# Kernel tuning notes

Hardware: AMD Instinct MI355X
Metric: run time of the kernel (lower is better)

## Reference

```python
import jax, jax.numpy as jnp
import numpy as np
import math

CHUNK = 32
NS_STEPS = 5
MAX_GNORM = 10.0


def _normalize(x, eps=1e-12):
    n = jnp.linalg.norm(x, axis=-1, keepdims=True)
    return x / jnp.maximum(n, eps)


def _poly(x):  # poly_degree = 2: [x, x^2] / sqrt(2)
    return jnp.concatenate([x, x * x], axis=-1) / math.sqrt(2.0)


def _ns5(G):
    # Muon-style Newton-Schulz orthogonalization (quintic, 5 steps)
    a, b, c = 3.4445, -4.7750, 2.0315
    t = G.shape[0] > G.shape[1]
    X = G.T if t else G
    X = X / (jnp.linalg.norm(X) + 1e-7)
    for _ in range(NS_STEPS):
        A = X @ X.T
        B = b * A + c * (A @ A)
        X = a * X + B @ X
    return X.T if t else X


def _clip_mean(g):
    # per-sample grad-norm clipping to MAX_GNORM, then mean over samples
    n = g.shape[0]
    norms = jnp.maximum(jnp.linalg.norm(g.reshape(n, -1), axis=1), 1e-8)
    scale = jnp.maximum(norms / MAX_GNORM, 1.0)
    return jnp.mean(g / scale.reshape((n,) + (1,) * (g.ndim - 1)), axis=0)


def _mem_fwd(W0, W1, z):  # MemoryMLP depth=2, gelu (exact) between layers
    return jax.nn.gelu(z @ W0, approximate=False) @ W1


def setup_inputs() -> dict:
    key = jax.random.key(0)
    ks = jax.random.split(key, 16)
    B, S, D, M, P, H = 2, 1024, 2048, 512, 1024, 2048
    w = lambda k, shape, fan_in: jax.random.normal(k, shape, jnp.float32) / np.float32(np.sqrt(fan_in))
    return {
        "x": jax.random.normal(ks[0], (B, S, D), jnp.float32),
        "Wk": w(ks[1], (M, D), D),
        "Wv": w(ks[2], (M, D), D),
        "Wq": w(ks[3], (M, D), D),
        "Wout": w(ks[4], (D, M), M),
        "w_lr": w(ks[5], (1, D), D), "b_lr": jnp.full((1,), -4.0, jnp.float32),
        "w_mom": w(ks[6], (1, D), D), "b_mom": jnp.full((1,), 1.0, jnp.float32),
        "w_dec": w(ks[7], (1, D), D), "b_dec": jnp.full((1,), -3.0, jnp.float32),
        "w_gate": w(ks[8], (1, D), D), "b_gate": jnp.full((1,), -1.0, jnp.float32),
        "Wmem0": w(ks[9], (P, H), P),
        "Wmem1": w(ks[10], (H, P), H),
        "Wmemout": w(ks[11], (P, M), P),
        "Wvexp": w(ks[12], (M, P), M),
    }


def reference(x, Wk, Wv, Wq, Wout, w_lr, b_lr, w_mom, b_mom, w_dec, b_dec,
              w_gate, b_gate, Wmem0, Wmem1, Wmemout, Wvexp):
    # Inference path (torch.is_grad_enabled() == False): chunked ATLAS update.
    B, S, D = x.shape
    NC = S // CHUNK

    k = _normalize(x @ Wk.T)          # (B,S,M)
    v = x @ Wv.T                       # (B,S,M)
    q = _normalize(x @ Wq.T)          # (B,S,M)
    kp = _poly(k)                      # (B,S,P)
    qp = _poly(q)                      # (B,S,P)
    vexp = v @ Wvexp                   # v_expand: (B,S,P)

    gate = lambda w, b: jax.nn.sigmoid(jnp.einsum('bsd,od->bso', x, w) + b)
    lr, mom, dec, og = gate(w_lr, b_lr), gate(w_mom, b_mom), gate(w_dec, b_dec), gate(w_gate, b_gate)

    cmean = lambda t: t[..., 0].reshape(B, NC, CHUNK).mean(axis=(0, 2))  # per-chunk scalar
    lr_c, mom_c, dec_c = cmean(lr), cmean(mom), cmean(dec)

    chunks = lambda t: t.reshape(B, NC, CHUNK, t.shape[-1]).transpose(1, 0, 2, 3)  # (NC,B,C,F)
    qc, kc, vc = chunks(qp), chunks(kp), chunks(vexp)

    def loss_fn(params, kk, vv):  # ||M(k) - v||^2 per sample
        W0_, W1_ = params
        pred = jax.nn.gelu(kk @ W0_, approximate=False) @ W1_
        return jnp.sum((pred - vv) ** 2)

    grad_fn = jax.vmap(jax.grad(loss_fn), in_axes=((None, None), 0, 0))

    def step(carry, xs):
        W0, W1, S0, S1 = carry
        qch, kch, vch, lrc, momc, decc = xs
        retr = _mem_fwd(W0, W1, qch) @ Wmemout  # retrieve with pre-update params: (B,C,M)
        kf = kch.reshape(-1, kch.shape[-1])
        vf = vch.reshape(-1, vch.shape[-1])
        g0, g1 = grad_fn((W0, W1), kf, vf)      # per-sample grads
        g0, g1 = _clip_mean(g0), _clip_mean(g1)
        s0 = momc * S0 - lrc * g0                # surprise momentum
        s1 = momc * S1 - lrc * g1
        W0n = (1.0 - decc) * W0 + _ns5(s0) * lrc # forget gate + orthogonalized step
        W1n = (1.0 - decc) * W1 + _ns5(s1) * lrc
        return (W0n, W1n, s0, s1), retr

    init = (Wmem0, Wmem1, jnp.zeros_like(Wmem0), jnp.zeros_like(Wmem1))
    _, retrs = jax.lax.scan(step, init, (qc, kc, vc, lr_c, mom_c, dec_c))
    retrieved = retrs.transpose(1, 0, 2, 3).reshape(B, S, -1)  # (B,S,M)
    delta = retrieved @ Wout.T
    return x + delta * og
```

## Files before the change

kernel.cpp:

```cpp
#include <hip/hip_runtime.h>


typedef unsigned short us;
typedef __attribute__((ext_vector_type(8))) short s16x8;
typedef __attribute__((ext_vector_type(8))) unsigned short u16x8;
typedef __attribute__((ext_vector_type(4))) float f32x4;

#define MKP 72

__device__ __forceinline__ float gelu_f(float x) {
  return 0.5f * x * (1.0f + erff(x * 0.70710678118654752f));
}
__device__ __forceinline__ float gelu_grad_f(float x) {
  float cdf = 0.5f * (1.0f + erff(x * 0.70710678118654752f));
  float pdf = 0.3989422804014327f * expf(-0.5f * x * x);
  return cdf + x * pdf;
}
__device__ __forceinline__ float sigmoid_f(float x) { return 1.0f / (1.0f + expf(-x)); }

__device__ __forceinline__ us f2bf(float f) {
  union { float f; unsigned u; } v; v.f = f;
  unsigned r = (v.u + 0x7FFFu + ((v.u >> 16) & 1u)) >> 16;
  return (us)r;
}
__device__ __forceinline__ float bf2f(us h) {
  union { unsigned u; float f; } v; v.u = ((unsigned)h) << 16;
  return v.f;
}
__device__ __forceinline__ int cm_map(int n) {
  return ((n & 1023) >> 5) * 64 + (n >> 10) * 32 + (n & 31);
}
__device__ __forceinline__ size_t pf_off(int r, int k, int KB) {
  return ((size_t)(r >> 4) * KB + (k >> 5)) * 512 + ((k >> 3) & 3) * 128 + (r & 15) * 8 + (k & 7);
}

__device__ __forceinline__ float block_reduce_sum(float v, float* red) {
  int t = threadIdx.x;
  red[t] = v; __syncthreads();
  for (int s = blockDim.x >> 1; s > 0; s >>= 1) {
    if (t < s) red[t] += red[t + s];
    __syncthreads();
  }
  float r = red[0];
  __syncthreads();
  return r;
}

__device__ __forceinline__ void gemm_pk(const us* __restrict__ A,
                                        const us* __restrict__ B, int KB,
                                        int lane, int m0, int n0,
                                        f32x4 (&acc)[4][4]) {
  const us* am[4];
  const us* bm[4];
#pragma unroll
  for (int q = 0; q < 4; ++q) {
    am[q] = A + (size_t)((m0 >> 4) + q) * KB * 512 + lane * 8;
    bm[q] = B + (size_t)((n0 >> 4) + q) * KB * 512 + lane * 8;
  }
#pragma unroll
  for (int i = 0; i < 4; ++i)
#pragma unroll
    for (int j = 0; j < 4; ++j) acc[i][j] = (f32x4){0.f, 0.f, 0.f, 0.f};
  u16x8 a0[4], b0[4], a1[4], b1[4];
#pragma unroll
  for (int q = 0; q < 4; ++q) {
    a0[q] = *(const u16x8*)(am[q]);
    b0[q] = *(const u16x8*)(bm[q]);
    a1[q] = *(const u16x8*)(am[q] + 512);
    b1[q] = *(const u16x8*)(bm[q] + 512);
  }
  for (int kb = 0; kb < KB; kb += 2) {
#pragma unroll
    for (int mi = 0; mi < 4; ++mi)
#pragma unroll
      for (int ni = 0; ni < 4; ++ni)
        acc[mi][ni] = __builtin_amdgcn_mfma_f32_16x16x32_bf16(
            (s16x8)a0[mi], (s16x8)b0[ni], acc[mi][ni], 0, 0, 0);
    if (kb + 2 < KB) {
#pragma unroll
      for (int q = 0; q < 4; ++q) {
        a0[q] = *(const u16x8*)(am[q] + (size_t)(kb + 2) * 512);
        b0[q] = *(const u16x8*)(bm[q] + (size_t)(kb + 2) * 512);
      }
    }
#pragma unroll
    for (int mi = 0; mi < 4; ++mi)
#pragma unroll
      for (int ni = 0; ni < 4; ++ni)
        acc[mi][ni] = __builtin_amdgcn_mfma_f32_16x16x32_bf16(
            (s16x8)a1[mi], (s16x8)b1[ni], acc[mi][ni], 0, 0, 0);
    if (kb + 3 < KB) {
#pragma unroll
      for (int q = 0; q < 4; ++q) {
        a1[q] = *(const u16x8*)(am[q] + (size_t)(kb + 3) * 512);
        b1[q] = *(const u16x8*)(bm[q] + (size_t)(kb + 3) * 512);
      }
    }
  }
}

template<int EPI, int TM, int TN>
__global__ __launch_bounds__(256)
void mgp_k(const us* __restrict__ Aq, const us* __restrict__ Bq,
           us* __restrict__ Cq, us* __restrict__ C2q, const us* __restrict__ Eq,
           int K, int N, float c1, float c2,
           long sA, long sB, long sC, long sE) {
  __shared__ __align__(16) us ct[4 * 64 * 72];
  const int tid = threadIdx.x;
  const int wave = tid >> 6, lane = tid & 63;
  const int l15 = lane & 15, l4 = lane >> 4;
  const int wm = (wave >> 1) * 64, wn = (wave & 1) * 64;
  const int TPB = TM * TN;
  const int t = blockIdx.x;
  const int bz = t / TPB;
  const int ti = t - bz * TPB;
  const int m0 = (ti / TN) * 128 + wm;
  const int n0 = (ti % TN) * 128 + wn;

  const us* A = Aq + (size_t)bz * sA;
  const us* B = Bq + (size_t)bz * sB;
  us* C = Cq + (size_t)bz * sC;
  us* C2 = C2q + (size_t)bz * sC;
  const us* E = Eq + (size_t)bz * sE;
  const int KB = K >> 5;

  f32x4 acc[4][4];
  gemm_pk(A, B, KB, lane, m0, n0, acc);

  us* cw = ct + wave * 64 * 72;
#pragma unroll
  for (int mi = 0; mi < 4; ++mi)
#pragma unroll
    for (int i = 0; i < 4; ++i)
#pragma unroll
      for (int ni = 0; ni < 4; ++ni)
        cw[(mi * 16 + l4 * 4 + i) * 72 + ni * 16 + l15] = f2bf(acc[mi][ni][i]);

  if constexpr (EPI == 20 || EPI == 21) {
    const int KC = N >> 5;
#pragma unroll
    for (int q = 0; q < 8; ++q) {
      u16x8 v = *(const u16x8*)&cw[lane * 72 + q * 8];
      size_t off = pf_off(m0 + lane, n0 + q * 8, KC);
      if constexpr (EPI == 21) {
        u16x8 e = *(const u16x8*)(E + off);
        u16x8 o;
#pragma unroll
        for (int w = 0; w < 8; ++w) o[w] = f2bf(c1 * bf2f(v[w]) + c2 * bf2f(e[w]));
        *(u16x8*)(C + off) = o;
      } else {
        *(u16x8*)(C + off) = v;
      }
    }
  } else if constexpr (EPI == 23) {
#pragma unroll
    for (int q = 0; q < 8; ++q) {
      size_t off = pf_off(m0 + lane, n0 + q * 8, 64);
      u16x8 v = *(const u16x8*)&cw[lane * 72 + q * 8];
      u16x8 e = *(const u16x8*)(E + off);
      u16x8 o;
#pragma unroll
      for (int w = 0; w < 8; ++w) o[w] = f2bf(bf2f(v[w]) + c1 * bf2f(e[w]));
      *(u16x8*)&cw[lane * 72 + q * 8] = o;
      *(u16x8*)(C + off) = o;
    }
#pragma unroll
    for (int q = 0; q < 8; ++q) {
      u16x8 o;
#pragma unroll
      for (int w = 0; w < 8; ++w) o[w] = cw[(q * 8 + w) * 72 + lane];
      size_t offT = pf_off(n0 + lane, m0 + q * 8, 32);
      *(u16x8*)(C2 + offT) = o;
    }
  } else {
#pragma unroll
    for (int q = 0; q < 8; ++q) {
      size_t off = pf_off(m0 + lane, n0 + q * 8, 64);
      u16x8 v = *(const u16x8*)&cw[lane * 72 + q * 8];
      u16x8 e = *(const u16x8*)(E + off);
      u16x8 o;
#pragma unroll
      for (int w = 0; w < 8; ++w) o[w] = f2bf(bf2f(v[w]) + c1 * bf2f(e[w]));
      *(u16x8*)(C + (size_t)(m0 + lane) * 2048 + n0 + q * 8) = o;
    }
  }
}

template<int EPI, int TM, int TN>
static void mgp(hipStream_t st, const us* A, const us* B, us* C, us* C2,
                const us* E, int K, int N, float c1, float c2,
                long sA, long sB, long sC, long sE) {
  dim3 g(TM * TN * 2), b(256);
  hipLaunchKernelGGL((mgp_k<EPI, TM, TN>), g, b, 0, st, A, B, C, C2, E,
                     K, N, c1, c2, sA, sB, sC, sE);
}

template<int EPI>
__device__ __forceinline__ void epilogue(f32x4 (&acc)[4][4], int m0, int n0,
    int l15, int l4, void* Cq, void* C2, const void* Eq,
    const float* FX, const float* OG, const float* cp, int cidx,
    int ldc, int lde, float c1, float c2) {
#pragma unroll
  for (int mi = 0; mi < 4; ++mi) {
#pragma unroll
    for (int i = 0; i < 4; ++i) {
      int grow = m0 + mi * 16 + l4 * 4 + i;
#pragma unroll
      for (int ni = 0; ni < 4; ++ni) {
        int col = n0 + ni * 16 + l15;
        float v = acc[mi][ni][i];
        if constexpr (EPI == 5) {
          ((us*)Cq)[(size_t)grow * ldc + col] = f2bf(v);
        } else if constexpr (EPI == 7) {
          ((float*)Cq)[(size_t)grow * ldc + col] = v;
        } else if constexpr (EPI == 8) {
          ((us*)Cq)[(size_t)grow * ldc + col] = f2bf(gelu_f(v));
          if (m0 >= 64)
            ((float*)C2)[(size_t)(grow - 64) * ldc + col] = gelu_grad_f(v);
        } else if constexpr (EPI == 9) {
          if (m0 < 64)
            ((us*)Cq)[(size_t)grow * ldc + col] = f2bf(v);
          else
            ((us*)Cq)[(size_t)grow * ldc + col] =
                f2bf(2.0f * (v - ((const float*)Eq)[(size_t)(grow - 64) * lde + col]));
        } else if constexpr (EPI == 13) {
          ((float*)Cq)[(size_t)grow * ldc + col] =
              v * ((const float*)Eq)[(size_t)grow * lde + col];
        } else if constexpr (EPI == 14) {
          float* C = (float*)Cq;
          float old = C[(size_t)grow * ldc + col];
          C[(size_t)grow * ldc + col] = cp[cidx * 3 + 1] * old - cp[cidx * 3 + 0] * v;
        } else if constexpr (EPI == 15) {
          ((float*)Cq)[(size_t)grow * ldc + col] =
              FX[(size_t)grow * ldc + col] + v * OG[grow];
        } else if constexpr (EPI == 17) {
          int crow = cm_map(grow);
          ((float*)Cq)[(size_t)crow * ldc + col] = v;
        }
      }
    }
  }
}

template<int EPI, int TA, int DUAL, int AG>
__device__ __forceinline__ void mg_body(const us* __restrict__ A0,
    const us* __restrict__ A2, const us* __restrict__ B,
    void* __restrict__ Cq, void* __restrict__ C2, const void* __restrict__ Eq,
    const float* __restrict__ FX, const float* __restrict__ OG,
    const float* __restrict__ cp, int cidx, int m0, int n0,
    int K, int lda, int ldb, int ldc, int lde, float c1, float c2,
    us* As, us* Bs, int t) {
  const us* A = A0;
  if constexpr (DUAL) { if (m0 >= 64) A = A2; }
  const int mA0 = DUAL ? (m0 & 63) : m0;
  const int l15 = t & 15, l4 = t >> 4;

  f32x4 acc[4][4];
#pragma unroll
  for (int i = 0; i < 4; ++i)
#pragma unroll
    for (int j = 0; j < 4; ++j) acc[i][j] = (f32x4){0.f, 0.f, 0.f, 0.f};

  const int srw = t >> 3;
  const int sck = (t & 7) * 8;

  u16x8 ra[8], rb[8];
  auto LDA = [&](int k0) {
#pragma unroll
    for (int p = 0; p < 8; ++p) {
      if constexpr (TA == 0) {
        int row = srw + p * 8;
        int srow;
        if constexpr (AG) srow = cm_map(m0 + row); else srow = mA0 + row;
        ra[p] = *(const u16x8*)(A + (size_t)srow * lda + k0 + sck);
      } else {
        ra[p] = *(const u16x8*)(A + (size_t)(k0 + srw + p * 8) * lda + mA0 + sck);
      }
    }
  };
  auto LDB = [&](int k0) {
#pragma unroll
    for (int p = 0; p < 8; ++p)
      rb[p] = *(const u16x8*)(B + (size_t)(n0 + srw + p * 8) * ldb + k0 + sck);
  };

  LDA(0); LDB(0);
  for (int k0 = 0; k0 < K; k0 += 64) {
    if constexpr (TA == 0) {
#pragma unroll
      for (int p = 0; p < 8; ++p)
        *(u16x8*)&As[(srw + p * 8) * MKP + sck] = ra[p];
    } else {
#pragma unroll
      for (int p = 0; p < 8; ++p) {
        int kk = srw + p * 8;
#pragma unroll
        for (int j = 0; j < 8; ++j) As[(sck + j) * MKP + kk] = ra[p][j];
      }
    }
#pragma unroll
    for (int p = 0; p < 8; ++p)
      *(u16x8*)&Bs[(srw + p * 8) * MKP + sck] = rb[p];
    if (k0 + 64 < K) { LDA(k0 + 64); LDB(k0 + 64); }
#pragma unroll
    for (int ks = 0; ks < 2; ++ks) {
      s16x8 af[4], bf[4];
#pragma unroll
      for (int mi = 0; mi < 4; ++mi)
        af[mi] = *(const s16x8*)&As[(mi * 16 + l15) * MKP + ks * 32 + l4 * 8];
#pragma unroll
      for (int ni = 0; ni < 4; ++ni)
        bf[ni] = *(const s16x8*)&Bs[(ni * 16 + l15) * MKP + ks * 32 + l4 * 8];
#pragma unroll
      for (int mi = 0; mi < 4; ++mi)
#pragma unroll
        for (int ni = 0; ni < 4; ++ni)
          acc[mi][ni] = __builtin_amdgcn_mfma_f32_16x16x32_bf16(af[mi], bf[ni], acc[mi][ni], 0, 0, 0);
    }
  }

  epilogue<EPI>(acc, m0, n0, l15, l4, Cq, C2, Eq, FX, OG, cp, cidx,
                ldc, lde, c1, c2);
}

template<int EPI, int TA, int DUAL, int AG>
__global__ __launch_bounds__(64)
void mg_k(const us* __restrict__ Aq, const us* __restrict__ A2,
          const us* __restrict__ Bq, void* __restrict__ Cq,
          void* __restrict__ C2, const void* __restrict__ Eq,
          const float* __restrict__ FX, const float* __restrict__ OG,
          const float* __restrict__ cp, int cidx,
          int M, int N, int K, int lda, int ldb, int ldc, int lde,
          float c1, float c2) {
  __shared__ __align__(16) us As[64 * MKP];
  __shared__ __align__(16) us Bs[64 * MKP];
  mg_body<EPI, TA, DUAL, AG>(Aq, A2, Bq, Cq, C2, Eq, FX, OG, cp, cidx,
                             blockIdx.y * 64, blockIdx.x * 64, K, lda, ldb,
                             ldc, lde, c1, c2, As, Bs, threadIdx.x);
}

template<int EPI, int TA = 0, int DUAL = 0, int AG = 0>
static void mg(hipStream_t st, const us* A, const us* A2, const us* B,
               void* C, void* C2, const void* E,
               const float* FX, const float* OG, const float* cp, int cidx,
               int M, int N, int K, int lda, int ldb, int ldc, int lde,
               float c1 = 0.f, float c2 = 0.f) {
  dim3 g(N / 64, M / 64, 1), b(64);
  hipLaunchKernelGGL((mg_k<EPI, TA, DUAL, AG>), g, b, 0, st, A, A2, B, C, C2, E,
                     FX, OG, cp, cidx, M, N, K, lda, ldb, ldc, lde, c1, c2);
}

__global__ __launch_bounds__(64)
void mg2_k(const us* __restrict__ kp_c, const us* __restrict__ dhT,
           float* __restrict__ S0, const us* __restrict__ habk,
           const us* __restrict__ rbwT, float* __restrict__ S1,
           const float* __restrict__ cp, int c) {
  __shared__ __align__(16) us As[64 * MKP];
  __shared__ __align__(16) us Bs[64 * MKP];
  int bid = blockIdx.x;
  if (bid < 512) {
    int m0 = (bid >> 5) * 64, n0 = (bid & 31) * 64;
    mg_body<14, 1, 0, 0>(kp_c, nullptr, dhT, S0, nullptr, nullptr,
                         nullptr, nullptr, cp, c, m0, n0,
                         64, 1024, 64, 2048, 0, 0.f, 0.f, As, Bs, threadIdx.x);
  } else {
    int b2 = bid - 512;
    int m0 = (b2 >> 4) * 64, n0 = (b2 & 15) * 64;
    mg_body<14, 1, 0, 0>(habk, nullptr, rbwT, S1, nullptr, nullptr,
                         nullptr, nullptr, cp, c, m0, n0,
                         64, 2048, 64, 1024, 0, 0.f, 0.f, As, Bs, threadIdx.x);
  }
}

__global__ void wt2_k(const float* __restrict__ dh, const float* __restrict__ w0inv,
                      us* __restrict__ dhT, const us* __restrict__ prg,
                      const float* __restrict__ w1inv, us* __restrict__ rbwT) {
  __shared__ float tile[32][33];
  int bid = blockIdx.x;
  int tx = threadIdx.x, ty = threadIdx.y;
  int c0, r0, ldin;
  const float* wv;
  us* outp;
  bool f32in;
  const void* in;
  if (bid < 128) {
    in = dh; wv = w0inv; outp = dhT; ldin = 2048; f32in = true;
    c0 = (bid & 63) * 32; r0 = (bid >> 6) * 32;
  } else {
    int b2 = bid - 128;
    in = prg; wv = w1inv; outp = rbwT; ldin = 1024; f32in = false;
    c0 = (b2 & 31) * 32; r0 = (b2 >> 5) * 32;
  }
#pragma unroll
  for (int j = 0; j < 4; ++j) {
    int r = r0 + ty + 8 * j, cc = c0 + tx;
    float v = f32in ? ((const float*)in)[(size_t)r * ldin + cc]
                    : bf2f(((const us*)in)[(size_t)r * ldin + cc]);
    tile[ty + 8 * j][tx] = v * wv[r];
  }
  __syncthreads();
#pragma unroll
  for (int j = 0; j < 4; ++j)
    outp[(size_t)(c0 + ty + 8 * j) * 64 + r0 + tx] = f2bf(tile[tx][ty + 8 * j]);
}

__global__ void scalepk2_k(const float* __restrict__ S0, const float* __restrict__ S1,
                           const float* __restrict__ inv01,
                           us* __restrict__ XP, us* __restrict__ XTP) {
  __shared__ float tile[32][33];
  const long SB2c = 2097152;
  int z = blockIdx.z;
  float s = inv01[z];
  int tx = threadIdx.x, ty = threadIdx.y;
  int r0, c0;
  const float* S;
  if (z == 0) { S = S0; c0 = blockIdx.x * 32; r0 = blockIdx.y * 32; }
  else        { S = S1; r0 = blockIdx.x * 32; c0 = blockIdx.y * 32; }
  int C = (z == 0) ? 2048 : 1024;
#pragma unroll
  for (int j = 0; j < 4; ++j)
    tile[ty + 8 * j][tx] = S[(size_t)(r0 + ty + 8 * j) * C + c0 + tx] * s;
  __syncthreads();
  us* xp = XP + (size_t)z * SB2c;
  us* xt = XTP + (size_t)z * SB2c;
  int t = ty * 32 + tx;
  if (t < 128) {
    int rh = t >> 2, cc = t & 3;
    u16x8 v;
#pragma unroll
    for (int e = 0; e < 8; ++e) v[e] = f2bf(tile[rh][cc * 8 + e]);
    if (z == 0) {
      *(u16x8*)(xp + pf_off(r0 + rh, c0 + cc * 8, 64)) = v;
    } else {
      *(u16x8*)(xt + pf_off(r0 + rh, c0 + cc * 8, 32)) = v;
    }
  } else {
    int ch = (t - 128) >> 2, rc = (t - 128) & 3;
    u16x8 v;
#pragma unroll
    for (int e = 0; e < 8; ++e) v[e] = f2bf(tile[rc * 8 + e][ch]);
    if (z == 0) {
      *(u16x8*)(xt + pf_off(c0 + ch, r0 + rc * 8, 32)) = v;
    } else {
      *(u16x8*)(xp + pf_off(c0 + ch, r0 + rc * 8, 64)) = v;
    }
  }
}


__global__ __launch_bounds__(256) void conv_k(const float* __restrict__ in,
                                              us* __restrict__ out, int n) {
  for (int i = blockIdx.x * 256 + threadIdx.x; i < n; i += gridDim.x * 256)
    out[i] = f2bf(in[i]);
}

__global__ void tconv_k(const float* __restrict__ in, us* __restrict__ out, int R, int C) {
  __shared__ float tile[32][33];
  int c0 = blockIdx.x * 32, r0 = blockIdx.y * 32;
  int tx = threadIdx.x, ty = threadIdx.y;
#pragma unroll
  for (int j = 0; j < 4; ++j)
    tile[ty + 8 * j][tx] = in[(size_t)(r0 + ty + 8 * j) * C + c0 + tx];
  __syncthreads();
#pragma unroll
  for (int j = 0; j < 4; ++j)
    out[(size_t)(c0 + ty + 8 * j) * R + r0 + tx] = f2bf(tile[tx][ty + 8 * j]);
}


__global__ __launch_bounds__(256) void polynorm2_k(const float* __restrict__ lin,
                                                   us* __restrict__ outp) {
  __shared__ float red[256];
  int n = blockIdx.x, t = threadIdx.x;
  int rowp = cm_map(n);
  float s = 0.f;
  for (int f = t; f < 512; f += 256) { float v = lin[(size_t)n * 512 + f]; s += v * v; }
  float tot = block_reduce_sum(s, red);
  float sc = 1.0f / fmaxf(sqrtf(tot), 1e-12f);
  const float is2 = 0.70710678118654752f;
  for (int f = t; f < 512; f += 256) {
    float v = lin[(size_t)n * 512 + f] * sc;
    outp[(size_t)rowp * 1024 + f] = f2bf(v * is2);
    outp[(size_t)rowp * 1024 + 512 + f] = f2bf(v * v * is2);
  }
}

__global__ __launch_bounds__(256) void gates_k(const float* __restrict__ x,
    const float* __restrict__ wlr, const float* __restrict__ blr,
    const float* __restrict__ wmom, const float* __restrict__ bmom,
    const float* __restrict__ wdec, const float* __restrict__ bdec,
    const float* __restrict__ wgate, const float* __restrict__ bgate,
    float* __restrict__ lrv, float* __restrict__ momv,
    float* __restrict__ decv, float* __restrict__ og) {
  __shared__ float red[256];
  int n = blockIdx.x, t = threadIdx.x;
  float s0 = 0.f, s1 = 0.f, s2 = 0.f, s3 = 0.f;
  for (int d = t; d < 2048; d += 256) {
    float xv = x[(size_t)n * 2048 + d];
    s0 += xv * wlr[d]; s1 += xv * wmom[d]; s2 += xv * wdec[d]; s3 += xv * wgate[d];
  }
  float r0 = block_reduce_sum(s0, red);
  float r1 = block_reduce_sum(s1, red);
  float r2 = block_reduce_sum(s2, red);
  float r3 = block_reduce_sum(s3, red);
  if (t == 0) {
    lrv[n] = sigmoid_f(r0 + blr[0]);
    momv[n] = sigmoid_f(r1 + bmom[0]);
    decv[n] = sigmoid_f(r2 + bdec[0]);
    og[n] = sigmoid_f(r3 + bgate[0]);
  }
}

__global__ void chunk_means_k(const float* __restrict__ lrv, const float* __restrict__ momv,
                              const float* __restrict__ decv, float* __restrict__ cp) {
  int c = blockIdx.x, t = threadIdx.x;
  int n = ((t >> 5) << 10) + c * 32 + (t & 31);
  float a = lrv[n], b = momv[n], d = decv[n];
  for (int off = 32; off > 0; off >>= 1) {
    a += __shfl_down(a, off);
    b += __shfl_down(b, off);
    d += __shfl_down(d, off);
  }
  if (t == 0) {
    cp[c * 3 + 0] = a * (1.f / 64.f);
    cp[c * 3 + 1] = b * (1.f / 64.f);
    cp[c * 3 + 2] = d * (1.f / 64.f);
  }
}

__global__ __launch_bounds__(256) void sampnorm2_k(const us* __restrict__ kp_b,
                                                   const float* __restrict__ dh,
                                                   const us* __restrict__ hab,
                                                   const us* __restrict__ pr,
                                                   float* __restrict__ w0inv,
                                                   float* __restrict__ w1inv, int c) {
  __shared__ float red[256];
  int i = blockIdx.x, t = threadIdx.x;
  int row = c * 64 + i;
  float sk = 0.f, sr = 0.f, sdh = 0.f, sa = 0.f;
  for (int p = t; p < 1024; p += 256) {
    float v = bf2f(kp_b[(size_t)row * 1024 + p]); sk += v * v;
    v = bf2f(pr[(size_t)(64 + i) * 1024 + p]); sr += v * v;
  }
  for (int h = t; h < 2048; h += 256) {
    float v = dh[(size_t)i * 2048 + h]; sdh += v * v;
    v = bf2f(hab[(size_t)(64 + i) * 2048 + h]); sa += v * v;
  }
  float tk = block_reduce_sum(sk, red);
  float tdh = block_reduce_sum(sdh, red);
  float ta = block_reduce_sum(sa, red);
  float tr = block_reduce_sum(sr, red);
  if (t == 0) {
    float n0 = fmaxf(sqrtf(tk) * sqrtf(tdh), 1e-8f);
    w0inv[i] = 1.0f / (64.0f * fmaxf(n0 * 0.1f, 1.0f));
    float n1 = fmaxf(sqrtf(ta) * sqrtf(tr), 1e-8f);
    w1inv[i] = 1.0f / (64.0f * fmaxf(n1 * 0.1f, 1.0f));
  }
}

__global__ __launch_bounds__(256) void frob2_k(const float* __restrict__ s0,
                                               const float* __restrict__ s1, int n,
                                               float* __restrict__ parts) {
  __shared__ float red[256];
  const float* s = blockIdx.z ? s1 : s0;
  float acc = 0.f;
  for (int i = blockIdx.x * 256 + threadIdx.x; i < n; i += gridDim.x * 256) {
    float v = s[i]; acc += v * v;
  }
  float r = block_reduce_sum(acc, red);
  if (threadIdx.x == 0) parts[blockIdx.z * 256 + blockIdx.x] = r;
}

__global__ __launch_bounds__(256) void frob_fin2_k(const float* __restrict__ parts,
                                                   float* __restrict__ inv) {
  __shared__ float red[256];
  float r = block_reduce_sum(parts[blockIdx.x * 256 + threadIdx.x], red);
  if (threadIdx.x == 0) inv[blockIdx.x] = 1.0f / (sqrtf(r) + 1e-7f);
}

__global__ void wupd0_k(float* __restrict__ W0, const us* __restrict__ X,
                        us* __restrict__ W0bT, const float* __restrict__ cp, int c) {
  __shared__ float tl[32][33];
  float lr = cp[c * 3 + 0], om = 1.0f - cp[c * 3 + 2];
  int c0 = blockIdx.x * 32, r0 = blockIdx.y * 32;
  int tx = threadIdx.x, ty = threadIdx.y;
#pragma unroll
  for (int j = 0; j < 4; ++j) {
    int r = r0 + ty + 8 * j, h = c0 + tx;
    size_t idx = (size_t)r * 2048 + h;
    float v = om * W0[idx] + lr * bf2f(X[idx]);
    W0[idx] = v;
    tl[ty + 8 * j][tx] = v;
  }
  __syncthreads();
#pragma unroll
  for (int j = 0; j < 4; ++j)
    W0bT[(size_t)(c0 + ty + 8 * j) * 1024 + r0 + tx] = f2bf(tl[tx][ty + 8 * j]);
}

__global__ void wupd1_k(float* __restrict__ W1, const us* __restrict__ X2,
                        us* __restrict__ W1b, us* __restrict__ W1bT,
                        const float* __restrict__ cp, int c) {
  __shared__ float tX[32][33];
  __shared__ float t2[32][33];
  float lr = cp[c * 3 + 0], om = 1.0f - cp[c * 3 + 2];
  int h0 = blockIdx.x * 32, p0 = blockIdx.y * 32;
  int tx = threadIdx.x, ty = threadIdx.y;
#pragma unroll
  for (int j = 0; j < 4; ++j)
    tX[ty + 8 * j][tx] = bf2f(X2[(size_t)(p0 + ty + 8 * j) * 2048 + h0 + tx]);
  __syncthreads();
#pragma unroll
  for (int j = 0; j < 4; ++j) {
    int h = h0 + ty + 8 * j, p = p0 + tx;
    size_t idx = (size_t)h * 1024 + p;
    float v = om * W1[idx] + lr * tX[tx][ty + 8 * j];
    W1[idx] = v;
    W1b[idx] = f2bf(v);
    t2[tx][ty + 8 * j] = v;
  }
  __syncthreads();
#pragma unroll
  for (int j = 0; j < 4; ++j)
    W1bT[(size_t)(p0 + ty + 8 * j) * 2048 + h0 + tx] = f2bf(t2[ty + 8 * j][tx]);
}


extern "C" void kernel_launch(void* const* d_in, const int* in_sizes, int n_in,
                              void* d_out, int out_size, void* d_ws, size_t ws_size,
                              hipStream_t stream) {
  const float* x = (const float*)d_in[0];
  const float* Wk = (const float*)d_in[1];
  const float* Wv = (const float*)d_in[2];
  const float* Wq = (const float*)d_in[3];
  const float* Wout = (const float*)d_in[4];
  const float* w_lr = (const float*)d_in[5];
  const float* b_lr = (const float*)d_in[6];
  const float* w_mom = (const float*)d_in[7];
  const float* b_mom = (const float*)d_in[8];
  const float* w_dec = (const float*)d_in[9];
  const float* b_dec = (const float*)d_in[10];
  const float* w_gate = (const float*)d_in[11];
  const float* b_gate = (const float*)d_in[12];
  const float* Wmem0 = (const float*)d_in[13];
  const float* Wmem1 = (const float*)d_in[14];
  const float* Wmemout = (const float*)d_in[15];
  const float* Wvexp = (const float*)d_in[16];
  float* out = (float*)d_out;
  (void)n_in; (void)in_sizes; (void)out_size;

  const long F = 1048576;
  const long BIG = 2097152;
  const long SB2 = 2097152, SB1 = 1048576;
  float* ws = (float*)d_ws;
  if (ws_size < (size_t)25043464 * sizeof(float)) return;

  us* kp_b   = (us*)ws;
  us* qp_b   = (us*)(ws + F);
  float* vexp = ws + 2 * F;
  float* W0  = ws + 4 * F;
  float* W1  = ws + 6 * F;
  float* S0  = ws + 8 * F;
  float* S1  = ws + 10 * F;
  us* XPong  = (us*)(ws + 12 * F);
  us* XTPong = (us*)(ws + 14 * F);
  us* XPing  = (us*)(ws + 16 * F);
  us* AP     = (us*)(ws + 18 * F);
  float* SCR = ws + 19 * F;
  us* XTPing = (us*)(ws + 20 * F);
  us* BP     = (us*)(ws + 22 * F);
  us* W0bT   = (us*)(ws + 20 * F);
  us* W1bT   = (us*)(ws + 21 * F);
  us* W1b    = (us*)(ws + 22 * F);
  us* WmoT   = (us*)(ws + 23 * F);
  us* retrv  = (us*)(ws + 23 * F + 262144);
  float* smal = ws + 23 * F + 262144 + 524288;
  float* og   = smal;
  float* lrv  = og + 2048;
  float* momv = lrv + 2048;
  float* decv = momv + 2048;
  float* cpb  = decv + 2048;
  float* w0inv = cpb + 128;
  float* w1inv = w0inv + 64;
  float* parts = w1inv + 64;
  float* inv01 = parts + 512;

  us* xb   = XPong;
  us* Wkb  = XTPong;
  us* Wqb  = XTPong + 1048576;
  us* Wvb  = XTPong + 2097152;
  us* vlin = XPing;
  us* WvexpT = XPing + 1048576;
  us* Woutb = AP;
  float* lin = SCR;
  us* hab   = (us*)SCR;
  float* gp = SCR + 131072;
  us* pr    = (us*)(SCR + 262144);
  float* dh = SCR + 327680;
  us* dhT   = (us*)(SCR + 458752);
  us* rbwT  = (us*)(SCR + 524288);
  us* Xfin  = XPong;

  const float NSa = 3.4445f, NSb = -4.7750f, NSc = 2.0315f;

  hipMemcpyAsync(W0, Wmem0, (size_t)BIG * 4, hipMemcpyDeviceToDevice, stream);
  hipMemcpyAsync(W1, Wmem1, (size_t)BIG * 4, hipMemcpyDeviceToDevice, stream);
  hipMemsetAsync(S0, 0, (size_t)BIG * 4, stream);
  hipMemsetAsync(S1, 0, (size_t)BIG * 4, stream);
  hipLaunchKernelGGL(tconv_k, dim3(64, 32), dim3(32, 8), 0, stream, Wmem0, W0bT, 1024, 2048);
  hipLaunchKernelGGL(conv_k, dim3(1024), dim3(256), 0, stream, Wmem1, W1b, (int)BIG);
  hipLaunchKernelGGL(tconv_k, dim3(32, 64), dim3(32, 8), 0, stream, Wmem1, W1bT, 2048, 1024);
  hipLaunchKernelGGL(tconv_k, dim3(16, 32), dim3(32, 8), 0, stream, Wmemout, WmoT, 1024, 512);
  hipLaunchKernelGGL(tconv_k, dim3(32, 16), dim3(32, 8), 0, stream, Wvexp, WvexpT, 512, 1024);
  hipLaunchKernelGGL(conv_k, dim3(2048), dim3(256), 0, stream, x, xb, 2048 * 2048);
  hipLaunchKernelGGL(conv_k, dim3(512), dim3(256), 0, stream, Wk, Wkb, 512 * 2048);
  hipLaunchKernelGGL(conv_k, dim3(512), dim3(256), 0, stream, Wq, Wqb, 512 * 2048);
  hipLaunchKernelGGL(conv_k, dim3(512), dim3(256), 0, stream, Wv, Wvb, 512 * 2048);

  mg<7>(stream, xb, nullptr, Wkb, lin, nullptr, nullptr, nullptr, nullptr, nullptr, 0,
        2048, 512, 2048, 2048, 2048, 512, 0);
  hipLaunchKernelGGL(polynorm2_k, dim3(2048), dim3(256), 0, stream, lin, kp_b);
  mg<7>(stream, xb, nullptr, Wqb, lin, nullptr, nullptr, nullptr, nullptr, nullptr, 0,
        2048, 512, 2048, 2048, 2048, 512, 0);
  hipLaunchKernelGGL(polynorm2_k, dim3(2048), dim3(256), 0, stream, lin, qp_b);
  mg<5>(stream, xb, nullptr, Wvb, vlin, nullptr, nullptr, nullptr, nullptr, nullptr, 0,
        2048, 512, 2048, 2048, 2048, 512, 0);
  mg<17>(stream, vlin, nullptr, WvexpT, vexp, nullptr, nullptr, nullptr, nullptr, nullptr, 0,
         2048, 1024, 512, 512, 512, 1024, 0);

  hipLaunchKernelGGL(gates_k, dim3(2048), dim3(256), 0, stream, x,
                     w_lr, b_lr, w_mom, b_mom, w_dec, b_dec, w_gate, b_gate,
                     lrv, momv, decv, og);
  hipLaunchKernelGGL(chunk_means_k, dim3(32), dim3(64), 0, stream, lrv, momv, decv, cpb);

  for (int c = 0; c < 32; ++c) {
    const us* kp_c = kp_b + (size_t)c * 64 * 1024;
    const us* qp_c = qp_b + (size_t)c * 64 * 1024;
    const float* vexp_c = vexp + (size_t)c * 64 * 1024;
    mg<8, 0, 1>(stream, qp_c, kp_c, W0bT, hab, gp, nullptr, nullptr, nullptr, nullptr, 0,
                128, 2048, 1024, 1024, 1024, 2048, 0);
    mg<9>(stream, hab, nullptr, W1bT, pr, nullptr, vexp_c, nullptr, nullptr, nullptr, 0,
          128, 1024, 2048, 2048, 2048, 1024, 1024);
    mg<5>(stream, pr, nullptr, WmoT, retrv + (size_t)c * 64 * 512, nullptr, nullptr,
          nullptr, nullptr, nullptr, 0, 64, 512, 1024, 1024, 1024, 512, 0);
    mg<13>(stream, pr + 64 * 1024, nullptr, W1b, dh, nullptr, gp, nullptr, nullptr, nullptr, 0,
           64, 2048, 1024, 1024, 1024, 2048, 2048);
    hipLaunchKernelGGL(sampnorm2_k, dim3(64), dim3(256), 0, stream,
                       kp_b, dh, hab, pr, w0inv, w1inv, c);
    hipLaunchKernelGGL(wt2_k, dim3(192), dim3(32, 8), 0, stream,
                       dh, w0inv, dhT, pr + 64 * 1024, w1inv, rbwT);
    hipLaunchKernelGGL(mg2_k, dim3(1024), dim3(64), 0, stream,
                       kp_c, dhT, S0, hab + 64 * 2048, rbwT, S1, cpb, c);

    hipLaunchKernelGGL(frob2_k, dim3(256, 1, 2), dim3(256), 0, stream, S0, S1, (int)BIG, parts);
    hipLaunchKernelGGL(frob_fin2_k, dim3(2), dim3(256), 0, stream, parts, inv01);
    hipLaunchKernelGGL(scalepk2_k, dim3(64, 32, 2), dim3(32, 8), 0, stream,
                       S0, S1, inv01, XPing, XTPing);

    us* xpA[2] = {XPing, XPong};
    us* xtA[2] = {XTPing, XTPong};
    int cur = 0;
    for (int it = 0; it < 5; ++it) {
      const us* XPc = xpA[cur];
      const us* XTPc = xtA[cur];
      int nxt = cur ^ 1;
      mgp<20, 8, 8>(stream, XPc, XPc, AP, nullptr, nullptr, 2048, 1024,
                    0.f, 0.f, SB2, SB2, SB1, 0);
      mgp<21, 8, 8>(stream, AP, AP, BP, nullptr, AP, 1024, 1024,
                    NSc, NSb, SB1, SB1, SB1, SB1);
      if (it < 4) {
        mgp<23, 8, 16>(stream, BP, XTPc, xpA[nxt], xtA[nxt], XPc, 1024, 2048,
                       NSa, 0.f, SB1, SB2, SB2, SB2);
        cur = nxt;
      } else {
        mgp<24, 8, 16>(stream, BP, XTPc, Xfin, nullptr, XPc, 1024, 2048,
                       NSa, 0.f, SB1, SB2, SB2, SB2);
      }
    }
    hipLaunchKernelGGL(wupd0_k, dim3(64, 32), dim3(32, 8), 0, stream, W0, Xfin, W0bT, cpb, c);
    hipLaunchKernelGGL(wupd1_k, dim3(64, 32), dim3(32, 8), 0, stream, W1, Xfin + SB2, W1b, W1bT, cpb, c);
  }

  hipLaunchKernelGGL(conv_k, dim3(1024), dim3(256), 0, stream, Wout, Woutb, 2048 * 512);
  mg<15, 0, 0, 1>(stream, retrv, nullptr, Woutb, out, nullptr, nullptr, x, og, nullptr, 0,
                  2048, 2048, 512, 512, 512, 2048, 0);
}
```

Before: 15.34 ms.

## Fuse Frobenius norm into momentum GEMM epilogue and merge small per-chunk launches

The momentum-update GEMM epilogue now accumulates the sum of squares of the new surprise values and writes one partial per block, so the separate full-matrix Frobenius reduction pass over S0/S1 is gone. The two small retrieval and dh GEMMs are merged into one launch with block-index dispatch, and the two weight-update kernels are combined into one launch over a z dimension. The aim is to cut per-chunk launch count and a redundant read of the large momentum buffers, at the cost of a small extra reduction in the GEMM tail.

Measured after the change: 14.31 ms (median of 2 runs). 6.7% less time.

```diff
diff --git a/kernel.cpp b/kernel.cpp
--- a/kernel.cpp
+++ b/kernel.cpp
@@ -196,10 +196,11 @@
 }
 
 template<int EPI>
-__device__ __forceinline__ void epilogue(f32x4 (&acc)[4][4], int m0, int n0,
+__device__ __forceinline__ float epilogue(f32x4 (&acc)[4][4], int m0, int n0,
     int l15, int l4, void* Cq, void* C2, const void* Eq,
     const float* FX, const float* OG, const float* cp, int cidx,
     int ldc, int lde, float c1, float c2) {
+  float ssq = 0.f;
 #pragma unroll
   for (int mi = 0; mi < 4; ++mi) {
 #pragma unroll
@@ -229,7 +230,9 @@
         } else if constexpr (EPI == 14) {
           float* C = (float*)Cq;
           float old = C[(size_t)grow * ldc + col];
-          C[(size_t)grow * ldc + col] = cp[cidx * 3 + 1] * old - cp[cidx * 3 + 0] * v;
+          float nv = cp[cidx * 3 + 1] * old - cp[cidx * 3 + 0] * v;
+          C[(size_t)grow * ldc + col] = nv;
+          ssq += nv * nv;
         } else if constexpr (EPI == 15) {
           ((float*)Cq)[(size_t)grow * ldc + col] =
               FX[(size_t)grow * ldc + col] + v * OG[grow];
@@ -240,10 +243,11 @@
       }
     }
   }
+  return ssq;
 }
 
 template<int EPI, int TA, int DUAL, int AG>
-__device__ __forceinline__ void mg_body(const us* __restrict__ A0,
+__device__ __forceinline__ float mg_body(const us* __restrict__ A0,
     const us* __restrict__ A2, const us* __restrict__ B,
     void* __restrict__ Cq, void* __restrict__ C2, const void* __restrict__ Eq,
     const float* __restrict__ FX, const float* __restrict__ OG,
@@ -319,8 +323,8 @@
     }
   }
 
-  epilogue<EPI>(acc, m0, n0, l15, l4, Cq, C2, Eq, FX, OG, cp, cidx,
-                ldc, lde, c1, c2);
+  return epilogue<EPI>(acc, m0, n0, l15, l4, Cq, C2, Eq, FX, OG, cp, cidx,
+                       ldc, lde, c1, c2);
 }
 
 template<int EPI, int TA, int DUAL, int AG>
@@ -354,21 +358,43 @@
 void mg2_k(const us* __restrict__ kp_c, const us* __restrict__ dhT,
            float* __restrict__ S0, const us* __restrict__ habk,
            const us* __restrict__ rbwT, float* __restrict__ S1,
-           const float* __restrict__ cp, int c) {
+           const float* __restrict__ cp, int c, float* __restrict__ parts2) {
   __shared__ __align__(16) us As[64 * MKP];
   __shared__ __align__(16) us Bs[64 * MKP];
   int bid = blockIdx.x;
+  float ssq;
   if (bid < 512) {
     int m0 = (bid >> 5) * 64, n0 = (bid & 31) * 64;
-    mg_body<14, 1, 0, 0>(kp_c, nullptr, dhT, S0, nullptr, nullptr,
-                         nullptr, nullptr, cp, c, m0, n0,
-                         64, 1024, 64, 2048, 0, 0.f, 0.f, As, Bs, threadIdx.x);
+    ssq = mg_body<14, 1, 0, 0>(kp_c, nullptr, dhT, S0, nullptr, nullptr,
+                               nullptr, nullptr, cp, c, m0, n0,
+                               64, 1024, 64, 2048, 0, 0.f, 0.f, As, Bs, threadIdx.x);
   } else {
     int b2 = bid - 512;
     int m0 = (b2 >> 4) * 64, n0 = (b2 & 15) * 64;
-    mg_body<14, 1, 0, 0>(habk, nullptr, rbwT, S1, nullptr, nullptr,
-                         nullptr, nullptr, cp, c, m0, n0,
-                         64, 2048, 64, 1024, 0, 0.f, 0.f, As, Bs, threadIdx.x);
+    ssq = mg_body<14, 1, 0, 0>(habk, nullptr, rbwT, S1, nullptr, nullptr,
+                               nullptr, nullptr, cp, c, m0, n0,
+                               64, 2048, 64, 1024, 0, 0.f, 0.f, As, Bs, threadIdx.x);
+  }
+  for (int off = 32; off > 0; off >>= 1) ssq += __shfl_down(ssq, off);
+  if (threadIdx.x == 0) parts2[bid] = ssq;
+}
+
+__global__ __launch_bounds__(64)
+void mg34_k(const us* __restrict__ pr, const us* __restrict__ WmoT,
+            us* __restrict__ retrv_c, const us* __restrict__ W1b,
+            float* __restrict__ dh, const float* __restrict__ gp) {
+  __shared__ __align__(16) us As[64 * MKP];
+  __shared__ __align__(16) us Bs[64 * MKP];
+  int bid = blockIdx.x;
+  if (bid < 8) {
+    mg_body<5, 0, 0, 0>(pr, nullptr, WmoT, retrv_c, nullptr, nullptr,
+                        nullptr, nullptr, nullptr, 0, 0, bid * 64,
+                        1024, 1024, 1024, 512, 0, 0.f, 0.f, As, Bs, threadIdx.x);
+  } else {
+    int b2 = bid - 8;
+    mg_body<13, 0, 0, 0>(pr + 64 * 1024, nullptr, W1b, dh, nullptr, gp,
+                         nullptr, nullptr, nullptr, 0, 0, b2 * 64,
+                         1024, 1024, 1024, 2048, 2048, 0.f, 0.f, As, Bs, threadIdx.x);
   }
 }
 
@@ -558,71 +584,57 @@
   }
 }
 
-__global__ __launch_bounds__(256) void frob2_k(const float* __restrict__ s0,
-                                               const float* __restrict__ s1, int n,
-                                               float* __restrict__ parts) {
-  __shared__ float red[256];
-  const float* s = blockIdx.z ? s1 : s0;
-  float acc = 0.f;
-  for (int i = blockIdx.x * 256 + threadIdx.x; i < n; i += gridDim.x * 256) {
-    float v = s[i]; acc += v * v;
-  }
-  float r = block_reduce_sum(acc, red);
-  if (threadIdx.x == 0) parts[blockIdx.z * 256 + blockIdx.x] = r;
-}
-
-__global__ __launch_bounds__(256) void frob_fin2_k(const float* __restrict__ parts,
-                                                   float* __restrict__ inv) {
-  __shared__ float red[256];
-  float r = block_reduce_sum(parts[blockIdx.x * 256 + threadIdx.x], red);
-  if (threadIdx.x == 0) inv[blockIdx.x] = 1.0f / (sqrtf(r) + 1e-7f);
-}
-
-__global__ void wupd0_k(float* __restrict__ W0, const us* __restrict__ X,
-                        us* __restrict__ W0bT, const float* __restrict__ cp, int c) {
-  __shared__ float tl[32][33];
+__global__ __launch_bounds__(512) void frob_fin512_k(const float* __restrict__ parts2,
+                                                     float* __restrict__ inv) {
+  __shared__ float red[512];
+  int z = blockIdx.x;
+  float r = block_reduce_sum(parts2[z * 512 + threadIdx.x], red);
+  if (threadIdx.x == 0) inv[z] = 1.0f / (sqrtf(r) + 1e-7f);
+}
+
+__global__ void wupd01_k(float* __restrict__ W0, const us* __restrict__ X0,
+                         us* __restrict__ W0bT,
+                         float* __restrict__ W1, const us* __restrict__ X2,
+                         us* __restrict__ W1b, us* __restrict__ W1bT,
+                         const float* __restrict__ cp, int c) {
+  __shared__ float tA[32][33];
+  __shared__ float tB[32][33];
   float lr = cp[c * 3 + 0], om = 1.0f - cp[c * 3 + 2];
-  int c0 = blockIdx.x * 32, r0 = blockIdx.y * 32;
   int tx = threadIdx.x, ty = threadIdx.y;
-#pragma unroll
-  for (int j = 0; j < 4; ++j) {
-    int r = r0 + ty + 8 * j, h = c0 + tx;
-    size_t idx = (size_t)r * 2048 + h;
-    float v = om * W0[idx] + lr * bf2f(X[idx]);
-    W0[idx] = v;
-    tl[ty + 8 * j][tx] = v;
-  }
-  __syncthreads();
-#pragma unroll
-  for (int j = 0; j < 4; ++j)
-    W0bT[(size_t)(c0 + ty + 8 * j) * 1024 + r0 + tx] = f2bf(tl[tx][ty + 8 * j]);
-}
-
-__global__ void wupd1_k(float* __restrict__ W1, const us* __restrict__ X2,
-                        us* __restrict__ W1b, us* __restrict__ W1bT,
-                        const float* __restrict__ cp, int c) {
-  __shared__ float tX[32][33];
-  __shared__ float t2[32][33];
-  float lr = cp[c * 3 + 0], om = 1.0f - cp[c * 3 + 2];
-  int h0 = blockIdx.x * 32, p0 = blockIdx.y * 32;
-  int tx = threadIdx.x, ty = threadIdx.y;
-#pragma unroll
-  for (int j = 0; j < 4; ++j)
-    tX[ty + 8 * j][tx] = bf2f(X2[(size_t)(p0 + ty + 8 * j) * 2048 + h0 + tx]);
-  __syncthreads();
-#pragma unroll
-  for (int j = 0; j < 4; ++j) {
-    int h = h0 + ty + 8 * j, p = p0 + tx;
-    size_t idx = (size_t)h * 1024 + p;
-    float v = om * W1[idx] + lr * tX[tx][ty + 8 * j];
-    W1[idx] = v;
-    W1b[idx] = f2bf(v);
-    t2[tx][ty + 8 * j] = v;
-  }
-  __syncthreads();
-#pragma unroll
-  for (int j = 0; j < 4; ++j)
-    W1bT[(size_t)(p0 + ty + 8 * j) * 2048 + h0 + tx] = f2bf(t2[ty + 8 * j][tx]);
+  if (blockIdx.z == 0) {
+    int c0 = blockIdx.x * 32, r0 = blockIdx.y * 32;
+#pragma unroll
+    for (int j = 0; j < 4; ++j) {
+      int r = r0 + ty + 8 * j, h = c0 + tx;
+      size_t idx = (size_t)r * 2048 + h;
+      float v = om * W0[idx] + lr * bf2f(X0[idx]);
+      W0[idx] = v;
+      tA[ty + 8 * j][tx] = v;
+    }
+    __syncthreads();
+#pragma unroll
+    for (int j = 0; j < 4; ++j)
+      W0bT[(size_t)(c0 + ty + 8 * j) * 1024 + r0 + tx] = f2bf(tA[tx][ty + 8 * j]);
+  } else {
+    int h0 = blockIdx.x * 32, p0 = blockIdx.y * 32;
+#pragma unroll
+    for (int j = 0; j < 4; ++j)
+      tA[ty + 8 * j][tx] = bf2f(X2[(size_t)(p0 + ty + 8 * j) * 2048 + h0 + tx]);
+    __syncthreads();
+#pragma unroll
+    for (int j = 0; j < 4; ++j) {
+      int h = h0 + ty + 8 * j, p = p0 + tx;
+      size_t idx = (size_t)h * 1024 + p;
+      float v = om * W1[idx] + lr * tA[tx][ty + 8 * j];
+      W1[idx] = v;
+      W1b[idx] = f2bf(v);
+      tB[tx][ty + 8 * j] = v;
+    }
+    __syncthreads();
+#pragma unroll
+    for (int j = 0; j < 4; ++j)
+      W1bT[(size_t)(p0 + ty + 8 * j) * 2048 + h0 + tx] = f2bf(tB[ty + 8 * j][tx]);
+  }
 }
 
 
@@ -682,8 +694,8 @@
   float* cpb  = decv + 2048;
   float* w0inv = cpb + 128;
   float* w1inv = w0inv + 64;
-  float* parts = w1inv + 64;
-  float* inv01 = parts + 512;
+  float* parts2 = w1inv + 64;
+  float* inv01 = parts2 + 1024;
 
   us* xb   = XPong;
   us* Wkb  = XTPong;
@@ -741,19 +753,15 @@
                 128, 2048, 1024, 1024, 1024, 2048, 0);
     mg<9>(stream, hab, nullptr, W1bT, pr, nullptr, vexp_c, nullptr, nullptr, nullptr, 0,
           128, 1024, 2048, 2048, 2048, 1024, 1024);
-    mg<5>(stream, pr, nullptr, WmoT, retrv + (size_t)c * 64 * 512, nullptr, nullptr,
-          nullptr, nullptr, nullptr, 0, 64, 512, 1024, 1024, 1024, 512, 0);
-    mg<13>(stream, pr + 64 * 1024, nullptr, W1b, dh, nullptr, gp, nullptr, nullptr, nullptr, 0,
-           64, 2048, 1024, 1024, 1024, 2048, 2048);
+    hipLaunchKernelGGL(mg34_k, dim3(40), dim3(64), 0, stream,
+                       pr, WmoT, retrv + (size_t)c * 64 * 512, W1b, dh, gp);
     hipLaunchKernelGGL(sampnorm2_k, dim3(64), dim3(256), 0, stream,
                        kp_b, dh, hab, pr, w0inv, w1inv, c);
     hipLaunchKernelGGL(wt2_k, dim3(192), dim3(32, 8), 0, stream,
                        dh, w0inv, dhT, pr + 64 * 1024, w1inv, rbwT);
     hipLaunchKernelGGL(mg2_k, dim3(1024), dim3(64), 0, stream,
-                       kp_c, dhT, S0, hab + 64 * 2048, rbwT, S1, cpb, c);
-
-    hipLaunchKernelGGL(frob2_k, dim3(256, 1, 2), dim3(256), 0, stream, S0, S1, (int)BIG, parts);
-    hipLaunchKernelGGL(frob_fin2_k, dim3(2), dim3(256), 0, stream, parts, inv01);
+                       kp_c, dhT, S0, hab + 64 * 2048, rbwT, S1, cpb, c, parts2);
+    hipLaunchKernelGGL(frob_fin512_k, dim3(2), dim3(512), 0, stream, parts2, inv01);
     hipLaunchKernelGGL(scalepk2_k, dim3(64, 32, 2), dim3(32, 8), 0, stream,
                        S0, S1, inv01, XPing, XTPing);
 
@@ -777,8 +785,8 @@
                        NSa, 0.f, SB1, SB2, SB2, SB2);
       }
     }
-    hipLaunchKernelGGL(wupd0_k, dim3(64, 32), dim3(32, 8), 0, stream, W0, Xfin, W0bT, cpb, c);
-    hipLaunchKernelGGL(wupd1_k, dim3(64, 32), dim3(32, 8), 0, stream, W1, Xfin + SB2, W1b, W1bT, cpb, c);
+    hipLaunchKernelGGL(wupd01_k, dim3(64, 32, 2), dim3(32, 8), 0, stream,
+                       W0, Xfin, W0bT, W1, Xfin + SB2, W1b, W1bT, cpb, c);
   }
 
   hipLaunchKernelGGL(conv_k, dim3(1024), dim3(256), 0, stream, Wout, Woutb, 2048 * 512);
```
